# Performance work log

Measured on AMD Instinct MI355X. Metric: run time of the kernel, lower is better.

## Reference

```python
import jax, jax.numpy as jnp
import numpy as np

# Config: hidden=2048, num_heads=32, num_kv_heads=8, head_dim=64,
# compression_factor=2 -> r_hidden=1024, kv_dim=num_kv_heads*head_dim=512,
# num_neighbors=16, context_size=1 (no neighbor-repeat path, no cache concat).
H = 2048
NH = 32
NKV = 8
HD = H // NH          # 64
G = NH // NKV         # 4 key-value groups
RH = H // 2           # 1024
KVD = NKV * HD        # 512
B, S, N = 2, 2048, 16


def setup_inputs() -> dict:
    key = jax.random.key(0)
    k1, k2, k3, k4, k5, k6 = jax.random.split(key, 6)
    hidden_states = jax.random.normal(k1, (B, S, H), dtype=jnp.float32)
    retrieved_hidden_states = jax.random.normal(k2, (B, S, N, RH), dtype=jnp.float32)
    # nn.Linear weights are [out_features, in_features], trunc_normal std=in**-0.5
    Wq = jax.random.normal(k3, (NH * HD, H), dtype=jnp.float32) * (H ** -0.5)
    Wk = jax.random.normal(k4, (KVD, RH), dtype=jnp.float32) * (RH ** -0.5)
    Wv = jax.random.normal(k5, (KVD, RH), dtype=jnp.float32) * (RH ** -0.5)
    Wo = jax.random.normal(k6, (H, NH * HD), dtype=jnp.float32) * ((NH * HD) ** -0.5)
    return {
        "hidden_states": hidden_states,
        "retrieved_hidden_states": retrieved_hidden_states,
        "Wq": Wq,
        "Wk": Wk,
        "Wv": Wv,
        "Wo": Wo,
    }


def reference(hidden_states, retrieved_hidden_states, Wq, Wk, Wv, Wo):
    scaler = HD ** -0.5
    # queries: [B,S,H] -> [B,S,NKV,G,HD] (grouped-query layout; avoids
    # materializing the repeat_kv expansion while computing identical math)
    q = (jnp.einsum("bsh,eh->bse", hidden_states, Wq) * scaler)
    q = q.reshape(B, S, NKV, G, HD)
    # keys/values: [B,S,N,RH] -> [B,S,NKV,N,HD]
    k = jnp.einsum("bsnr,er->bsne", retrieved_hidden_states, Wk).reshape(B, S, N, NKV, HD)
    v = jnp.einsum("bsnr,er->bsne", retrieved_hidden_states, Wv).reshape(B, S, N, NKV, HD)
    k = jnp.moveaxis(k, 2, 3)  # [B,S,NKV,N,HD]
    v = jnp.moveaxis(v, 2, 3)
    # per-query attention over its own N retrieved neighbors
    scores = jnp.einsum("bsagd,bsand->bsagn", q, k)  # [B,S,NKV,G,N]
    attn = jax.nn.softmax(scores, axis=-1)
    out = jnp.einsum("bsagn,bsand->bsagd", attn, v)  # [B,S,NKV,G,HD]
    out = out.reshape(B, S, NH * HD)
    return jnp.einsum("bse,he->bsh", out, Wo)
```

## Files before the change

kernel.cpp:

```cpp
#include <hip/hip_runtime.h>
#include <hip/hip_bf16.h>
#include <cstdint>

#define AS1 __attribute__((address_space(1)))
#define AS3 __attribute__((address_space(3)))

typedef __attribute__((ext_vector_type(8))) __bf16 bf16x8;
typedef __attribute__((ext_vector_type(4))) float f32x4;

__device__ inline unsigned short f2bf(float f) {
    unsigned u = __float_as_uint(f);
    u += 0x7fffu + ((u >> 16) & 1);
    return (unsigned short)(u >> 16);
}
__device__ inline float bf_lo(unsigned u) { return __uint_as_float(u << 16); }
__device__ inline float bf_hi(unsigned u) { return __uint_as_float(u & 0xffff0000u); }

struct CastArgs {
    const float* s[6];
    unsigned short* d[6];
    long end[6];
};

__global__ void cast_all(CastArgs a, long total) {
    long e = ((long)blockIdx.x * blockDim.x + threadIdx.x) * 8;
    if (e >= total) return;
    int seg = 0;
#pragma unroll
    for (int i = 0; i < 5; i++) seg += (e >= a.end[seg]) ? 1 : 0;
    long base = seg ? a.end[seg - 1] : 0;
    long local = e - base;
    const float* src = a.s[seg] + local;
    float4 x = *(const float4*)src;
    float4 y = *(const float4*)(src + 4);
    ushort4 lo, hi;
    lo.x = f2bf(x.x); lo.y = f2bf(x.y); lo.z = f2bf(x.z); lo.w = f2bf(x.w);
    hi.x = f2bf(y.x); hi.y = f2bf(y.y); hi.z = f2bf(y.z); hi.w = f2bf(y.w);
    unsigned short* dst = a.d[seg] + local;
    *(ushort4*)dst = lo;
    *(ushort4*)(dst + 4) = hi;
}

template <int OUTF>
__global__ __launch_bounds__(256, 2)
void gemm_bt(const unsigned short* __restrict__ A, const unsigned short* __restrict__ B,
             void* __restrict__ Cv, int M, int N, int K, float scale) {
    __shared__ __align__(16) unsigned short As[128 * 32];
    __shared__ __align__(16) unsigned short Bs[128 * 32];

    const int t = threadIdx.x;
    const int w = t >> 6, lane = t & 63;
    const int bx = blockIdx.x, by = blockIdx.y;
    const int wr = w >> 1, wc = w & 1;
    const int quad = lane >> 4, lr = lane & 15;

    f32x4 acc[4][4] = {};

    const int srow = t >> 2;
    const int schunk = (t & 3) ^ ((srow >> 1) & 3);
    const unsigned short* gA = A + (size_t)(by * 128 + srow) * K + schunk * 8;
    const unsigned short* gB = B + (size_t)(bx * 128 + srow) * K + schunk * 8;
    char* aBase = (char*)As + w * 1024;
    char* bBase = (char*)Bs + w * 1024;

    const int rsw = (lr >> 1) & 3;
    const int aoff = quad ^ rsw;

    for (int k0 = 0; k0 < K; k0 += 32) {
        __builtin_amdgcn_global_load_lds((const AS1 void*)gA,
                                         (AS3 void*)aBase, 16, 0, 0);
        __builtin_amdgcn_global_load_lds((const AS1 void*)(gA + (size_t)64 * K),
                                         (AS3 void*)(aBase + 4096), 16, 0, 0);
        __builtin_amdgcn_global_load_lds((const AS1 void*)gB,
                                         (AS3 void*)bBase, 16, 0, 0);
        __builtin_amdgcn_global_load_lds((const AS1 void*)(gB + (size_t)64 * K),
                                         (AS3 void*)(bBase + 4096), 16, 0, 0);
        gA += 32; gB += 32;
        __syncthreads();

        bf16x8 af[4], bfr[4];
#pragma unroll
        for (int i = 0; i < 4; i++)
            af[i] = *(const bf16x8*)(As + (wr * 64 + i * 16 + lr) * 32 + aoff * 8);
#pragma unroll
        for (int j = 0; j < 4; j++)
            bfr[j] = *(const bf16x8*)(Bs + (wc * 64 + j * 16 + lr) * 32 + aoff * 8);
#pragma unroll
        for (int i = 0; i < 4; i++)
#pragma unroll
            for (int j = 0; j < 4; j++)
                acc[i][j] = __builtin_amdgcn_mfma_f32_16x16x32_bf16(
                    af[i], bfr[j], acc[i][j], 0, 0, 0);
        __syncthreads();
    }

#pragma unroll
    for (int i = 0; i < 4; i++) {
        int row0 = by * 128 + wr * 64 + i * 16 + quad * 4;
#pragma unroll
        for (int j = 0; j < 4; j++) {
            int col = bx * 128 + wc * 64 + j * 16 + lr;
#pragma unroll
            for (int r = 0; r < 4; r++) {
                float vv = acc[i][j][r] * scale;
                size_t idx = (size_t)(row0 + r) * N + col;
                if (OUTF) ((float*)Cv)[idx] = vv;
                else      ((unsigned short*)Cv)[idx] = f2bf(vv);
            }
        }
    }
}

__global__ __launch_bounds__(256, 4)
void attn_kernel(const unsigned short* __restrict__ q,
                 const unsigned short* __restrict__ kvb,
                 unsigned short* __restrict__ ao) {
    __shared__ __align__(16) unsigned short qs[4][4][72];
    __shared__ __align__(16) unsigned short ks[4][16][72];
    __shared__ __align__(16) unsigned short vs[4][16][72];
    __shared__ float ps[4][4][17];

    const int t = threadIdx.x, w = t >> 6, lane = t & 63;
    const int bs = blockIdx.x >> 1;
    const int kv = (blockIdx.x & 1) * 4 + w;

    if (lane < 32) {
        int g = lane >> 3, part = lane & 7;
        *(int4*)(&qs[w][g][part * 8]) =
            *(const int4*)(q + (size_t)bs * 2048 + kv * 256 + lane * 8);
    }
#pragma unroll
    for (int p = 0; p < 2; p++) {
        int n = p * 8 + (lane >> 3), part = lane & 7;
        size_t src = ((size_t)bs * 16 + n) * 1024 + kv * 64 + part * 8;
        *(int4*)(&ks[w][n][part * 8]) = *(const int4*)(kvb + src);
        *(int4*)(&vs[w][n][part * 8]) = *(const int4*)(kvb + src + 512);
    }
    __syncthreads();

    {
        const int g = lane & 3, n = lane >> 2;
        const unsigned short* qr = qs[w][g];
        const unsigned short* kr = ks[w][n];
        float s = 0.f;
#pragma unroll
        for (int d = 0; d < 64; d += 2) {
            unsigned uq = *(const unsigned*)(qr + d);
            unsigned uk = *(const unsigned*)(kr + d);
            s += bf_lo(uq) * bf_lo(uk) + bf_hi(uq) * bf_hi(uk);
        }
        float m = s;
#pragma unroll
        for (int off = 4; off < 64; off <<= 1) m = fmaxf(m, __shfl_xor(m, off));
        float e = __expf(s - m);
        float sum = e;
#pragma unroll
        for (int off = 4; off < 64; off <<= 1) sum += __shfl_xor(sum, off);
        ps[w][g][n] = e / sum;
    }
    __syncthreads();

    {
        const int g = lane & 3, d0 = (lane >> 2) * 4;
        float o0 = 0, o1 = 0, o2 = 0, o3 = 0;
#pragma unroll
        for (int n = 0; n < 16; n++) {
            float pv = ps[w][g][n];
            unsigned u0 = *(const unsigned*)(&vs[w][n][d0]);
            unsigned u1 = *(const unsigned*)(&vs[w][n][d0 + 2]);
            o0 += pv * bf_lo(u0); o1 += pv * bf_hi(u0);
            o2 += pv * bf_lo(u1); o3 += pv * bf_hi(u1);
        }
        unsigned r0 = ((unsigned)f2bf(o1) << 16) | f2bf(o0);
        unsigned r1 = ((unsigned)f2bf(o3) << 16) | f2bf(o2);
        uint2 rr = make_uint2(r0, r1);
        *(uint2*)(ao + (size_t)bs * 2048 + kv * 256 + g * 64 + d0) = rr;
    }
}

extern "C" void kernel_launch(void* const* d_in, const int* in_sizes, int n_in,
                              void* d_out, int out_size, void* d_ws, size_t ws_size,
                              hipStream_t stream) {
    (void)in_sizes; (void)n_in; (void)out_size; (void)ws_size;
    const float* hs = (const float*)d_in[0];
    const float* rh = (const float*)d_in[1];
    const float* Wq = (const float*)d_in[2];
    const float* Wk = (const float*)d_in[3];
    const float* Wv = (const float*)d_in[4];
    const float* Wo = (const float*)d_in[5];
    float* out = (float*)d_out;

    const int BS = 4096;
    const int H = 2048, RH = 1024, KVD = 512, NN = 16;

    char* ws = (char*)d_ws;
    auto alloc = [&](size_t elems) {
        unsigned short* p = (unsigned short*)ws;
        ws += elems * 2;
        return p;
    };
    unsigned short* hs_b = alloc((size_t)BS * H);
    unsigned short* rh_b = alloc((size_t)BS * NN * RH);
    unsigned short* wq_b = alloc((size_t)H * H);
    unsigned short* wk_b = alloc((size_t)KVD * RH);
    unsigned short* wv_b = alloc((size_t)KVD * RH);
    unsigned short* wo_b = alloc((size_t)H * H);
    unsigned short* q_b  = alloc((size_t)BS * H);
    unsigned short* kv_b = alloc((size_t)BS * NN * 2 * KVD);
    unsigned short* ao_b = hs_b;
    (void)wv_b;

    CastArgs ca;
    ca.s[0] = hs;  ca.d[0] = hs_b;
    ca.s[1] = rh;  ca.d[1] = rh_b;
    ca.s[2] = Wq;  ca.d[2] = wq_b;
    ca.s[3] = Wk;  ca.d[3] = wk_b;
    ca.s[4] = Wv;  ca.d[4] = wv_b;
    ca.s[5] = Wo;  ca.d[5] = wo_b;
    long sizes[6] = {(long)BS * H, (long)BS * NN * RH, (long)H * H,
                     (long)KVD * RH, (long)KVD * RH, (long)H * H};
    long acc = 0;
    for (int i = 0; i < 6; i++) { acc += sizes[i]; ca.end[i] = acc; }
    long total = acc;
    int cast_blocks = (int)((total / 8 + 255) / 256);
    cast_all<<<cast_blocks, 256, 0, stream>>>(ca, total);

    gemm_bt<0><<<dim3(H / 128, BS / 128), 256, 0, stream>>>(
        hs_b, wq_b, q_b, BS, H, H, 0.125f);
    gemm_bt<0><<<dim3((2 * KVD) / 128, (BS * NN) / 128), 256, 0, stream>>>(
        rh_b, wk_b, kv_b, BS * NN, 2 * KVD, RH, 1.0f);
    attn_kernel<<<BS * 2, 256, 0, stream>>>(q_b, kv_b, ao_b);
    gemm_bt<1><<<dim3(H / 128, BS / 128), 256, 0, stream>>>(
        ao_b, wo_b, out, BS, H, H, 1.0f);
}
```

Measured before the change: 757.2 us.

## Add double-buffered 256x256 GEMM for KV projection and remap blocks across XCDs

Adds a new 512-thread GEMM kernel with 256x256 tiles, K-step 64, double-buffered LDS, staged async global-to-LDS loads interleaved with MFMA phases, and s_setprio around the MFMA bursts. It replaces the 128x128 kernel for the large KV projection (M=65536). Both GEMM kernels also remap block IDs so consecutive tiles are spread across the 8 XCDs, aiming for better L2 locality. The larger tile roughly doubles data reuse per byte loaded. In exchange it uses more LDS and registers, which can lower occupancy, and the hand-placed waitcnt/barrier scheduling is fragile.

```diff
diff --git a/kernel.cpp b/kernel.cpp
--- a/kernel.cpp
+++ b/kernel.cpp
@@ -50,7 +50,11 @@
 
     const int t = threadIdx.x;
     const int w = t >> 6, lane = t & 63;
-    const int bx = blockIdx.x, by = blockIdx.y;
+    const int nbx = gridDim.x;
+    int id = blockIdx.y * nbx + blockIdx.x;
+    const int nwg = nbx * gridDim.y;
+    if ((nwg & 7) == 0) { const int cpx = nwg >> 3; id = (id & 7) * cpx + (id >> 3); }
+    const int bx = id % nbx, by = id / nbx;
     const int wr = w >> 1, wc = w & 1;
     const int quad = lane >> 4, lr = lane & 15;
 
@@ -109,6 +113,121 @@
             }
         }
     }
+}
+
+__global__ __launch_bounds__(512, 2)
+void gemm256_bt(const unsigned short* __restrict__ A, const unsigned short* __restrict__ B,
+                unsigned short* __restrict__ C, int M, int N, int K, float scale) {
+    __shared__ __align__(16) unsigned short As[2][256][64];
+    __shared__ __align__(16) unsigned short Bs[2][256][64];
+    (void)M;
+
+    const int tid = threadIdx.x;
+    const int w = tid >> 6, lane = tid & 63;
+    const int quad = lane >> 4, lr = lane & 15;
+    const int wr = w >> 2, wc = w & 3;
+
+    const int nbx = gridDim.x;
+    int id = blockIdx.y * nbx + blockIdx.x;
+    const int cpx = (nbx * gridDim.y) >> 3;
+    id = (id & 7) * cpx + (id >> 3);
+    const int bx = id % nbx, by = id / nbx;
+
+    const int NT = K >> 6;
+
+    const int o0 = ((quad ^ (lr & 7))) * 8;
+    const int o1 = (((4 | quad) ^ (lr & 7))) * 8;
+
+    const int sr8 = tid >> 3;
+    const int sch = (tid & 7) ^ (sr8 & 7);
+    const unsigned short* gA = A + (size_t)(by * 256 + sr8) * K + sch * 8;
+    const unsigned short* gB = B + (size_t)(bx * 256 + sr8) * K + sch * 8;
+    char* lA = (char*)&As[0][0][0] + w * 1024;
+    char* lB = (char*)&Bs[0][0][0] + w * 1024;
+    const size_t rowK64 = (size_t)64 * K;
+
+    auto stage = [&](int bufX, int tt, int hid) {
+        if (tt >= NT) return;
+        const int hf = hid & 1;
+        const unsigned short* g = (hid < 2 ? gB : gA) + (size_t)hf * 128 * K + (size_t)tt * 64;
+        char* l = (hid < 2 ? lB : lA) + bufX * 32768 + hf * 16384;
+        __builtin_amdgcn_global_load_lds((const AS1 void*)g, (AS3 void*)l, 16, 0, 0);
+        __builtin_amdgcn_global_load_lds((const AS1 void*)(g + rowK64),
+                                         (AS3 void*)(l + 8192), 16, 0, 0);
+    };
+
+    f32x4 acc[8][4] = {};
+
+    stage(0, 0, 0); stage(0, 0, 1); stage(0, 0, 2); stage(0, 0, 3);
+    asm volatile("s_waitcnt vmcnt(4)" ::: "memory");
+    stage(1, 1, 0); stage(1, 1, 1); stage(1, 1, 2);
+    asm volatile("s_waitcnt vmcnt(6)" ::: "memory");
+    __builtin_amdgcn_s_barrier();
+
+    const int arow = wr * 128 + lr;
+    const int brow = wc * 64 + lr;
+
+    for (int t = 0; t < NT; ++t) {
+        const int buf = t & 1;
+        const unsigned short* Ab = &As[buf][0][0];
+        const unsigned short* Bb = &Bs[buf][0][0];
+        bf16x8 bfr[4][2], af[2][2];
+
+#define LDA(Q) \
+        af[0][0] = *(const bf16x8*)(Ab + (arow + (2*(Q))*16) * 64 + o0); \
+        af[0][1] = *(const bf16x8*)(Ab + (arow + (2*(Q))*16) * 64 + o1); \
+        af[1][0] = *(const bf16x8*)(Ab + (arow + (2*(Q)+1)*16) * 64 + o0); \
+        af[1][1] = *(const bf16x8*)(Ab + (arow + (2*(Q)+1)*16) * 64 + o1);
+
+#define MMA(Q) \
+        __builtin_amdgcn_s_barrier(); \
+        __builtin_amdgcn_s_setprio(1); \
+        _Pragma("unroll") \
+        for (int j = 0; j < 4; ++j) { \
+            acc[2*(Q)][j]   = __builtin_amdgcn_mfma_f32_16x16x32_bf16(af[0][0], bfr[j][0], acc[2*(Q)][j], 0, 0, 0); \
+            acc[2*(Q)][j]   = __builtin_amdgcn_mfma_f32_16x16x32_bf16(af[0][1], bfr[j][1], acc[2*(Q)][j], 0, 0, 0); \
+            acc[2*(Q)+1][j] = __builtin_amdgcn_mfma_f32_16x16x32_bf16(af[1][0], bfr[j][0], acc[2*(Q)+1][j], 0, 0, 0); \
+            acc[2*(Q)+1][j] = __builtin_amdgcn_mfma_f32_16x16x32_bf16(af[1][1], bfr[j][1], acc[2*(Q)+1][j], 0, 0, 0); \
+        } \
+        __builtin_amdgcn_s_setprio(0); \
+        __builtin_amdgcn_s_barrier();
+
+        LDA(0)
+#pragma unroll
+        for (int j = 0; j < 4; ++j) {
+            bfr[j][0] = *(const bf16x8*)(Bb + (brow + j * 16) * 64 + o0);
+            bfr[j][1] = *(const bf16x8*)(Bb + (brow + j * 16) * 64 + o1);
+        }
+        stage(buf ^ 1, t + 1, 3);
+        MMA(0)
+        LDA(1)
+        stage(buf, t + 2, 0);
+        MMA(1)
+        LDA(2)
+        stage(buf, t + 2, 1);
+        MMA(2)
+        LDA(3)
+        stage(buf, t + 2, 2);
+        if (t + 2 < NT) { asm volatile("s_waitcnt vmcnt(6)" ::: "memory"); }
+        else            { asm volatile("s_waitcnt vmcnt(0)" ::: "memory"); }
+        MMA(3)
+#undef LDA
+#undef MMA
+    }
+
+    const int crow0 = by * 256 + wr * 128 + quad * 4;
+    const int ccol0 = bx * 256 + wc * 64 + lr;
+#pragma unroll
+    for (int f = 0; f < 8; ++f)
+#pragma unroll
+        for (int j = 0; j < 4; ++j) {
+            const int col = ccol0 + j * 16;
+#pragma unroll
+            for (int r = 0; r < 4; ++r) {
+                size_t idx = (size_t)(crow0 + f * 16 + r) * N + col;
+                C[idx] = f2bf(acc[f][j][r] * scale);
+            }
+        }
 }
 
 __global__ __launch_bounds__(256, 4)
@@ -227,7 +346,7 @@
 
     gemm_bt<0><<<dim3(H / 128, BS / 128), 256, 0, stream>>>(
         hs_b, wq_b, q_b, BS, H, H, 0.125f);
-    gemm_bt<0><<<dim3((2 * KVD) / 128, (BS * NN) / 128), 256, 0, stream>>>(
+    gemm256_bt<<<dim3((2 * KVD) / 256, (BS * NN) / 256), 512, 0, stream>>>(
         rh_b, wk_b, kv_b, BS * NN, 2 * KVD, RH, 1.0f);
     attn_kernel<<<BS * 2, 256, 0, stream>>>(q_b, kv_b, ao_b);
     gemm_bt<1><<<dim3(H / 128, BS / 128), 256, 0, stream>>>(
```

Measured after the change: 730.5 us. 3.5% less time.
